# Kernel optimization log

Measured on AMD Instinct MI355X. Metric: run time of the kernel, lower is better.

## Reference

```python
import jax, jax.numpy as jnp
import numpy as np

N_CLASSES = 8  # hardcoded by the (-1, 8, 8) reshape in the original layer

def setup_inputs() -> dict:
    key = jax.random.key(0)
    k1, k2, k3, k4 = jax.random.split(key, 4)
    B, F, C, R = 16384, 128, N_CLASSES, 64
    x = jax.random.normal(k1, (B, F), dtype=jnp.float32)
    p = jax.random.uniform(k2, (B, C), dtype=jnp.float32)  # class-prob-like input
    W = jax.random.normal(k3, (F, C * C, R), dtype=jnp.float32) * 0.02
    b = jax.random.normal(k4, (C, C, R), dtype=jnp.float32) * 0.1
    return {"x": x, "p": p, "W": W, "b": b}

def reference(x, p, W, b):
    # x: (B, 128) features; p: (B, C) class probs; W: (128, C*C, R); b: (C, C, R)
    B = x.shape[0]
    C = b.shape[0]
    R = b.shape[-1]
    # per-annotator GEMM fused across all annotators: (B, C*C, R)
    logits = jnp.einsum('bf,fkr->bkr', x, W).reshape(B, C, C, R) + b[None]
    # row-softmax: softmax over the "predicted class" axis for each true class c
    M = jax.nn.softmax(logits, axis=2)  # (B, C, C, R)
    # batched dot: p (B,C) contracted against rows of each annotator matrix
    out = jnp.einsum('bc,bcdr->bdr', p, M)  # (B, C, R)
    # NOTE: original applies K.dropout(0.5) (training-mode); omitted for a
    # deterministic inference reference (identity at eval).
    return out
```

## Files before the change

kernel.cpp:

```cpp
#include <hip/hip_runtime.h>
#include <hip/hip_bf16.h>


#define B_ROWS   16384
#define F_DIM    128
#define NCOL     4096
#define OUT_STRIDE 512
#define LOG2E    1.44269504088896340736f

typedef __bf16 bf16x8 __attribute__((ext_vector_type(8)));
typedef float  f32x4  __attribute__((ext_vector_type(4)));

#define AS1(p) ((const __attribute__((address_space(1))) unsigned int*)(p))
#define AS3(p) ((__attribute__((address_space(3))) unsigned int*)(p))

__global__ void wconv_kernel(const float* __restrict__ W, __bf16* __restrict__ wf) {
    int f    = blockIdx.x * 256 + threadIdx.x;
    int lane = f & 63;
    int gf   = f >> 6;
    int kk   = gf & 3;
    int w    = (gf >> 2) & 7;
    int t    = (gf >> 5) & 3;
    int c    = gf >> 7;
    int l15  = lane & 15;
    int kbase = kk * 32 + (lane >> 4) * 8;
    int col   = c * 512 + (2 * t + (l15 >> 3)) * 64 + w * 8 + (l15 & 7);
    bf16x8 frag;
#pragma unroll
    for (int j = 0; j < 8; ++j)
        frag[j] = (__bf16)W[(kbase + j) * NCOL + col];
    *(bf16x8*)(wf + (size_t)f * 8) = frag;
}

__global__ __launch_bounds__(256, 4)
void fused_kernel(const float* __restrict__ x, const float* __restrict__ p,
                  const float* __restrict__ bias, const __bf16* __restrict__ wf,
                  float* __restrict__ out) {
    __shared__ __align__(16) char lds[32768];

    const int lane = threadIdx.x & 63;
    const int ww   = threadIdx.x >> 6;
    const int quad = lane >> 4;
    const int l15  = lane & 15;
    const int h    = l15 >> 3;
    const int q    = l15 & 7;
    const int w    = blockIdx.x >> 7;
    const int g    = blockIdx.x & 127;
    const int b0   = g * 128 + ww * 32;

    bf16x8 afr[2][4];
#pragma unroll
    for (int m = 0; m < 2; ++m) {
        const float* xr = x + (size_t)(b0 + m * 16 + l15) * F_DIM + quad * 8;
#pragma unroll
        for (int kk = 0; kk < 4; ++kk) {
            float4 lo = *(const float4*)(xr + kk * 32);
            float4 hi = *(const float4*)(xr + kk * 32 + 4);
            bf16x8 f;
            f[0] = (__bf16)lo.x; f[1] = (__bf16)lo.y;
            f[2] = (__bf16)lo.z; f[3] = (__bf16)lo.w;
            f[4] = (__bf16)hi.x; f[5] = (__bf16)hi.y;
            f[6] = (__bf16)hi.z; f[7] = (__bf16)hi.w;
            afr[m][kk] = f;
        }
    }

    float O[2][4][4] = {};

    {
        const __bf16* src = wf + (size_t)((ww * 8 + w) * 4) * 512;
#pragma unroll
        for (int kk = 0; kk < 4; ++kk)
            __builtin_amdgcn_global_load_lds(
                AS1(src + kk * 512 + lane * 8),
                AS3(lds + (ww * 4 + kk) * 1024), 16, 0, 0);
    }

#pragma unroll 1
    for (int c = 0; c < 8; ++c) {
        __syncthreads();

        if (c < 7) {
            const __bf16* src = wf + (size_t)((((c + 1) * 4 + ww) * 8 + w) * 4) * 512;
            char* dst = lds + ((c + 1) & 1) * 16384;
#pragma unroll
            for (int kk = 0; kk < 4; ++kk)
                __builtin_amdgcn_global_load_lds(
                    AS1(src + kk * 512 + lane * 8),
                    AS3(dst + (ww * 4 + kk) * 1024), 16, 0, 0);
        }

        float pvv[2][4];
#pragma unroll
        for (int m = 0; m < 2; ++m)
#pragma unroll
            for (int jj = 0; jj < 4; ++jj)
                pvv[m][jj] = p[(size_t)(b0 + m * 16 + quad * 4 + jj) * 8 + c];

        float bvl[4];
#pragma unroll
        for (int t = 0; t < 4; ++t)
            bvl[t] = bias[c * 512 + (2 * t + h) * 64 + w * 8 + q];

        f32x4 acc[2][4];
#pragma unroll
        for (int t = 0; t < 4; ++t) {
            f32x4 binit = {bvl[t], bvl[t], bvl[t], bvl[t]};
            acc[0][t] = binit;
            acc[1][t] = binit;
        }

        const char* buf = lds + (c & 1) * 16384;
#pragma unroll
        for (int kk = 0; kk < 4; ++kk)
#pragma unroll
            for (int t = 0; t < 4; ++t) {
                bf16x8 bfr = *(const bf16x8*)(buf + (t * 4 + kk) * 1024 + lane * 16);
                acc[0][t] = __builtin_amdgcn_mfma_f32_16x16x32_bf16(
                                afr[0][kk], bfr, acc[0][t], 0, 0, 0);
                acc[1][t] = __builtin_amdgcn_mfma_f32_16x16x32_bf16(
                                afr[1][kk], bfr, acc[1][t], 0, 0, 0);
            }

#pragma unroll
        for (int m = 0; m < 2; ++m) {
#pragma unroll
            for (int jj = 0; jj < 4; ++jj) {
                float e0 = __builtin_amdgcn_exp2f(acc[m][0][jj] * LOG2E);
                float e1 = __builtin_amdgcn_exp2f(acc[m][1][jj] * LOG2E);
                float e2 = __builtin_amdgcn_exp2f(acc[m][2][jj] * LOG2E);
                float e3 = __builtin_amdgcn_exp2f(acc[m][3][jj] * LOG2E);
                float s4 = (e0 + e1) + (e2 + e3);
                float s8 = s4 + __shfl_xor(s4, 8, 64);
                float scale = pvv[m][jj] * __builtin_amdgcn_rcpf(s8);
                O[m][0][jj] = __builtin_fmaf(e0, scale, O[m][0][jj]);
                O[m][1][jj] = __builtin_fmaf(e1, scale, O[m][1][jj]);
                O[m][2][jj] = __builtin_fmaf(e2, scale, O[m][2][jj]);
                O[m][3][jj] = __builtin_fmaf(e3, scale, O[m][3][jj]);
            }
        }
    }

#pragma unroll
    for (int m = 0; m < 2; ++m)
#pragma unroll
        for (int jj = 0; jj < 4; ++jj) {
            float* orow = out + (size_t)(b0 + m * 16 + quad * 4 + jj) * OUT_STRIDE
                          + h * 64 + w * 8 + q;
#pragma unroll
            for (int t = 0; t < 4; ++t)
                orow[t * 128] = O[m][t][jj];
        }
}

extern "C" void kernel_launch(void* const* d_in, const int* in_sizes, int n_in,
                              void* d_out, int out_size, void* d_ws, size_t ws_size,
                              hipStream_t stream) {
    const float* x    = (const float*)d_in[0];
    const float* p    = (const float*)d_in[1];
    const float* W    = (const float*)d_in[2];
    const float* bias = (const float*)d_in[3];
    float* out = (float*)d_out;
    __bf16* wf = (__bf16*)d_ws;

    wconv_kernel<<<dim3(256), dim3(256), 0, stream>>>(W, wf);
    fused_kernel<<<dim3(1024), dim3(256), 0, stream>>>(x, p, bias, wf, out);
}
```

Baseline: 112.1 us.

## Fold log2e into weights/bias, transpose bias, reorder MFMA/exp, nontemporal stores

The weight conversion kernel now pre-multiplies W by log2(e), and also writes a log2(e)-scaled, transposed copy of the bias into workspace. This removes the per-element multiply before exp2 in the fused kernel and makes the per-thread bias loads contiguous. The fused kernel issues its first LDS prefetch before converting x, and moves the next-stage prefetch after the bias load. It also computes the MFMA chain per column tile so exp2 can overlap with later MFMAs, and writes output with nontemporal stores. Scaling before bf16 rounding changes numerics slightly.

```diff
diff --git a/kernel.cpp b/kernel.cpp
--- a/kernel.cpp
+++ b/kernel.cpp
@@ -2,7 +2,6 @@
 #include <hip/hip_bf16.h>
 
 
-#define B_ROWS   16384
 #define F_DIM    128
 #define NCOL     4096
 #define OUT_STRIDE 512
@@ -14,7 +13,10 @@
 #define AS1(p) ((const __attribute__((address_space(1))) unsigned int*)(p))
 #define AS3(p) ((__attribute__((address_space(3))) unsigned int*)(p))
 
-__global__ void wconv_kernel(const float* __restrict__ W, __bf16* __restrict__ wf) {
+__global__ void wconv_kernel(const float* __restrict__ W,
+                             const float* __restrict__ bias,
+                             __bf16* __restrict__ wf,
+                             float* __restrict__ biasT) {
     int f    = blockIdx.x * 256 + threadIdx.x;
     int lane = f & 63;
     int gf   = f >> 6;
@@ -28,13 +30,18 @@
     bf16x8 frag;
 #pragma unroll
     for (int j = 0; j < 8; ++j)
-        frag[j] = (__bf16)W[(kbase + j) * NCOL + col];
+        frag[j] = (__bf16)(W[(kbase + j) * NCOL + col] * LOG2E);
     *(bf16x8*)(wf + (size_t)f * 8) = frag;
+
+    if (f < 4096) {
+        int c2 = f >> 9, r = (f >> 3) & 63, d = f & 7;
+        biasT[f] = bias[(c2 * 8 + d) * 64 + r] * LOG2E;
+    }
 }
 
 __global__ __launch_bounds__(256, 4)
 void fused_kernel(const float* __restrict__ x, const float* __restrict__ p,
-                  const float* __restrict__ bias, const __bf16* __restrict__ wf,
+                  const float* __restrict__ biasT, const __bf16* __restrict__ wf,
                   float* __restrict__ out) {
     __shared__ __align__(16) char lds[32768];
 
@@ -47,6 +54,15 @@
     const int w    = blockIdx.x >> 7;
     const int g    = blockIdx.x & 127;
     const int b0   = g * 128 + ww * 32;
+
+    {
+        const __bf16* src = wf + (size_t)((ww * 8 + w) * 4) * 512 + lane * 8;
+#pragma unroll
+        for (int kk = 0; kk < 4; ++kk)
+            __builtin_amdgcn_global_load_lds(
+                AS1(src + kk * 512),
+                AS3(lds + (ww * 4 + kk) * 1024), 16, 0, 0);
+    }
 
     bf16x8 afr[2][4];
 #pragma unroll
@@ -67,28 +83,9 @@
 
     float O[2][4][4] = {};
 
-    {
-        const __bf16* src = wf + (size_t)((ww * 8 + w) * 4) * 512;
-#pragma unroll
-        for (int kk = 0; kk < 4; ++kk)
-            __builtin_amdgcn_global_load_lds(
-                AS1(src + kk * 512 + lane * 8),
-                AS3(lds + (ww * 4 + kk) * 1024), 16, 0, 0);
-    }
-
 #pragma unroll 1
     for (int c = 0; c < 8; ++c) {
         __syncthreads();
-
-        if (c < 7) {
-            const __bf16* src = wf + (size_t)((((c + 1) * 4 + ww) * 8 + w) * 4) * 512;
-            char* dst = lds + ((c + 1) & 1) * 16384;
-#pragma unroll
-            for (int kk = 0; kk < 4; ++kk)
-                __builtin_amdgcn_global_load_lds(
-                    AS1(src + kk * 512 + lane * 8),
-                    AS3(dst + (ww * 4 + kk) * 1024), 16, 0, 0);
-        }
 
         float pvv[2][4];
 #pragma unroll
@@ -100,43 +97,51 @@
         float bvl[4];
 #pragma unroll
         for (int t = 0; t < 4; ++t)
-            bvl[t] = bias[c * 512 + (2 * t + h) * 64 + w * 8 + q];
+            bvl[t] = biasT[(c * 64 + w * 8 + q) * 8 + 2 * t + h];
 
-        f32x4 acc[2][4];
+        if (c < 7) {
+            const __bf16* src =
+                wf + (size_t)((((c + 1) * 4 + ww) * 8 + w) * 4) * 512 + lane * 8;
+            char* dst = lds + ((c + 1) & 1) * 16384;
 #pragma unroll
-        for (int t = 0; t < 4; ++t) {
-            f32x4 binit = {bvl[t], bvl[t], bvl[t], bvl[t]};
-            acc[0][t] = binit;
-            acc[1][t] = binit;
+            for (int kk = 0; kk < 4; ++kk)
+                __builtin_amdgcn_global_load_lds(
+                    AS1(src + kk * 512),
+                    AS3(dst + (ww * 4 + kk) * 1024), 16, 0, 0);
         }
 
         const char* buf = lds + (c & 1) * 16384;
+        f32x4 e[2][4];
 #pragma unroll
-        for (int kk = 0; kk < 4; ++kk)
+        for (int t = 0; t < 4; ++t) {
+            f32x4 a0 = {bvl[t], bvl[t], bvl[t], bvl[t]};
+            f32x4 a1 = a0;
 #pragma unroll
-            for (int t = 0; t < 4; ++t) {
+            for (int kk = 0; kk < 4; ++kk) {
                 bf16x8 bfr = *(const bf16x8*)(buf + (t * 4 + kk) * 1024 + lane * 16);
-                acc[0][t] = __builtin_amdgcn_mfma_f32_16x16x32_bf16(
-                                afr[0][kk], bfr, acc[0][t], 0, 0, 0);
-                acc[1][t] = __builtin_amdgcn_mfma_f32_16x16x32_bf16(
-                                afr[1][kk], bfr, acc[1][t], 0, 0, 0);
+                a0 = __builtin_amdgcn_mfma_f32_16x16x32_bf16(afr[0][kk], bfr, a0, 0, 0, 0);
+                a1 = __builtin_amdgcn_mfma_f32_16x16x32_bf16(afr[1][kk], bfr, a1, 0, 0, 0);
             }
+#pragma unroll
+            for (int jj = 0; jj < 4; ++jj) {
+                a0[jj] = __builtin_amdgcn_exp2f(a0[jj]);
+                a1[jj] = __builtin_amdgcn_exp2f(a1[jj]);
+            }
+            e[0][t] = a0;
+            e[1][t] = a1;
+        }
 
 #pragma unroll
         for (int m = 0; m < 2; ++m) {
 #pragma unroll
             for (int jj = 0; jj < 4; ++jj) {
-                float e0 = __builtin_amdgcn_exp2f(acc[m][0][jj] * LOG2E);
-                float e1 = __builtin_amdgcn_exp2f(acc[m][1][jj] * LOG2E);
-                float e2 = __builtin_amdgcn_exp2f(acc[m][2][jj] * LOG2E);
-                float e3 = __builtin_amdgcn_exp2f(acc[m][3][jj] * LOG2E);
-                float s4 = (e0 + e1) + (e2 + e3);
+                float s4 = (e[m][0][jj] + e[m][1][jj])
+                         + (e[m][2][jj] + e[m][3][jj]);
                 float s8 = s4 + __shfl_xor(s4, 8, 64);
                 float scale = pvv[m][jj] * __builtin_amdgcn_rcpf(s8);
-                O[m][0][jj] = __builtin_fmaf(e0, scale, O[m][0][jj]);
-                O[m][1][jj] = __builtin_fmaf(e1, scale, O[m][1][jj]);
-                O[m][2][jj] = __builtin_fmaf(e2, scale, O[m][2][jj]);
-                O[m][3][jj] = __builtin_fmaf(e3, scale, O[m][3][jj]);
+#pragma unroll
+                for (int t = 0; t < 4; ++t)
+                    O[m][t][jj] = __builtin_fmaf(e[m][t][jj], scale, O[m][t][jj]);
             }
         }
     }
@@ -149,7 +154,7 @@
                           + h * 64 + w * 8 + q;
 #pragma unroll
             for (int t = 0; t < 4; ++t)
-                orow[t * 128] = O[m][t][jj];
+                __builtin_nontemporal_store(O[m][t][jj], orow + t * 128);
         }
 }
 
@@ -161,8 +166,9 @@
     const float* W    = (const float*)d_in[2];
     const float* bias = (const float*)d_in[3];
     float* out = (float*)d_out;
-    __bf16* wf = (__bf16*)d_ws;
+    __bf16* wf    = (__bf16*)d_ws;
+    float*  biasT = (float*)((char*)d_ws + (1 << 20));
 
-    wconv_kernel<<<dim3(256), dim3(256), 0, stream>>>(W, wf);
-    fused_kernel<<<dim3(1024), dim3(256), 0, stream>>>(x, p, bias, wf, out);
+    wconv_kernel<<<dim3(256), dim3(256), 0, stream>>>(W, bias, wf, biasT);
+    fused_kernel<<<dim3(1024), dim3(256), 0, stream>>>(x, p, biasT, wf, out);
 }
```

After: 129.4 us. 15.4% more time.
